# Kernel tuning notes

Hardware: AMD Instinct MI355X
Metric: run time of the kernel (lower is better)

Reference implementation:

```python
import jax, jax.numpy as jnp
import numpy as np

DIM = 180
WS = 16        # window_size
OWS = 24       # overlap_win_size = int(16*0.5)+16
HEADS = 6
HD = DIM // HEADS
MLP_HID = DIM * 2
TABLE = (WS + OWS - 1) ** 2  # 1521
H = W = 256
B = 1


def layernorm(x, g, b, eps=1e-5):
    mu = x.mean(-1, keepdims=True)
    d = x - mu
    var = (d * d).mean(-1, keepdims=True)
    return g * d / jnp.sqrt(var + eps) + b


def setup_inputs() -> dict:
    key = jax.random.key(0)
    ks = jax.random.split(key, 12)
    std = 0.02
    inp = {
        'x': jax.random.normal(ks[0], (B, H * W, DIM), jnp.float32),
        'rpi': jax.random.randint(ks[1], (WS * WS, OWS * OWS), 0, TABLE, jnp.int32),
        'h': H,
        'w': W,
        'norm1_g': jnp.ones((DIM,), jnp.float32),
        'norm1_b': jnp.zeros((DIM,), jnp.float32),
        'q_w': jax.random.normal(ks[2], (DIM, DIM), jnp.float32) * std,
        'q_b': jnp.zeros((DIM,), jnp.float32),
        'kv_w': jax.random.normal(ks[3], (DIM, 2 * DIM), jnp.float32) * std,
        'kv_b': jnp.zeros((2 * DIM,), jnp.float32),
        'rpb_table': jax.random.normal(ks[4], (TABLE, HEADS), jnp.float32) * std,
        'proj_w': jax.random.normal(ks[5], (DIM, DIM), jnp.float32) * std,
        'proj_b': jnp.zeros((DIM,), jnp.float32),
        'norm2_g': jnp.ones((DIM,), jnp.float32),
        'norm2_b': jnp.zeros((DIM,), jnp.float32),
        'mlp_w1': jax.random.normal(ks[6], (DIM, MLP_HID), jnp.float32) * std,
        'mlp_b1': jnp.zeros((MLP_HID,), jnp.float32),
        'mlp_w2': jax.random.normal(ks[7], (MLP_HID, DIM), jnp.float32) * std,
        'mlp_b2': jnp.zeros((DIM,), jnp.float32),
    }
    return inp


def reference(x, rpi, h, w, norm1_g, norm1_b, q_w, q_b, kv_w, kv_b,
              rpb_table, proj_w, proj_b, norm2_g, norm2_b,
              mlp_w1, mlp_b1, mlp_w2, mlp_b2):
    b, L, c = x.shape
    ws, ows, heads = WS, OWS, HEADS
    d = c // heads
    scale = d ** -0.5
    pad = (ows - ws) // 2  # 4
    nh, nw = h // ws, w // ws
    nq, n = ws * ws, ows * ows
    b_ = b * nh * nw

    shortcut = x
    xn = layernorm(x, norm1_g, norm1_b)
    x_img = xn.reshape(b, h, w, c)

    q = x_img @ q_w + q_b                    # [b,h,w,c]
    kv = x_img @ kv_w + kv_b                 # [b,h,w,2c] (k | v)

    # window_partition for q -> [b_, nq, c]
    qw = q.reshape(b, nh, ws, nw, ws, c).transpose(0, 1, 3, 2, 4, 5)
    qw = qw.reshape(b_, nq, c)

    # nn.Unfold(kernel=ows, stride=ws, padding=pad) on kv -> overlapping windows
    kvp = jnp.pad(kv, ((0, 0), (pad, pad), (pad, pad), (0, 0)))
    rows = (jnp.arange(nh) * ws)[:, None] + jnp.arange(ows)   # [nh, ows]
    cols = (jnp.arange(nw) * ws)[:, None] + jnp.arange(ows)   # [nw, ows]
    t = kvp[:, rows]                         # [b, nh, ows, W+2p, 2c]
    t = t[:, :, :, cols]                     # [b, nh, ows, nw, ows, 2c]
    t = t.transpose(0, 1, 3, 2, 4, 5).reshape(b_, n, 2 * c)
    k_win, v_win = t[..., :c], t[..., c:]

    qh = qw.reshape(b_, nq, heads, d).transpose(0, 2, 1, 3) * scale
    kh = k_win.reshape(b_, n, heads, d).transpose(0, 2, 1, 3)
    vh = v_win.reshape(b_, n, heads, d).transpose(0, 2, 1, 3)

    attn = jnp.einsum('bhqd,bhkd->bhqk', qh, kh)              # [b_,heads,nq,n]
    bias = rpb_table[rpi.reshape(-1)].reshape(nq, n, heads).transpose(2, 0, 1)
    attn = jax.nn.softmax(attn + bias[None], axis=-1)
    out = jnp.einsum('bhqk,bhkd->bhqd', attn, vh)
    out = out.transpose(0, 2, 1, 3).reshape(b_, nq, c)

    # window_reverse -> [b, h*w, c]
    xo = out.reshape(b, nh, nw, ws, ws, c).transpose(0, 1, 3, 2, 4, 5)
    xo = xo.reshape(b, h * w, c)

    xo = xo @ proj_w + proj_b + shortcut
    xn2 = layernorm(xo, norm2_g, norm2_b)
    mlp = jax.nn.gelu(xn2 @ mlp_w1 + mlp_b1, approximate=False) @ mlp_w2 + mlp_b2
    return xo + mlp
```

## Files before the change

### kernel.cpp

```cpp
#include <hip/hip_runtime.h>
#include <hip/hip_bf16.h>
#include <stdint.h>

#define DIM 180
#define WS 16
#define OWS 24
#define HEADS 6
#define HD 30
#define MLP_HID 360
#define HH 256
#define WW 256
#define L (HH * WW)
#define NWIN 256
#define NQ 256
#define NK 576

#define KP1 192
#define KP2 384
#define NQKV 576

#define QSCALE 0.2633988734672831f
#define LOG2E 1.4426950408889634f

typedef float f4v __attribute__((ext_vector_type(4)));
typedef short s8v __attribute__((ext_vector_type(8)));
typedef short s4v __attribute__((ext_vector_type(4)));

static __device__ __forceinline__ short f2bf(float x) {
    union { __hip_bfloat16 h; short s; } u;
    u.h = __float2bfloat16(x);
    return u.s;
}
static __device__ __forceinline__ uint32_t pack_bf2(float lo, float hi) {
    union { __hip_bfloat162 h; uint32_t u; } u;
    u.h.x = __float2bfloat16(lo);
    u.h.y = __float2bfloat16(hi);
    return u.u;
}
static __device__ __forceinline__ float bflo(uint32_t u) {
    union { uint32_t i; float f; } c; c.i = u << 16; return c.f;
}
static __device__ __forceinline__ float bfhi(uint32_t u) {
    union { uint32_t i; float f; } c; c.i = u & 0xffff0000u; return c.f;
}

typedef __attribute__((address_space(1))) const unsigned int ga_u32;
typedef __attribute__((address_space(3))) unsigned int la_u32;
static __device__ __forceinline__ void gld16(const void* g, void* l) {
    __builtin_amdgcn_global_load_lds((ga_u32*)g, (la_u32*)l, 16, 0, 0);
}

__global__ __launch_bounds__(64) void ln_kernel(const float* __restrict__ x,
                                                const float* __restrict__ g,
                                                const float* __restrict__ b,
                                                __hip_bfloat16* __restrict__ out) {
    int row = blockIdx.x;
    int t = threadIdx.x;
    const float* xr = x + (size_t)row * DIM;
    float v0 = xr[t];
    float v1 = xr[t + 64];
    float v2 = (t < DIM - 128) ? xr[t + 128] : 0.f;
    float s = v0 + v1 + v2;
    #pragma unroll
    for (int o = 32; o > 0; o >>= 1) s += __shfl_down(s, o);
    s = __shfl(s, 0);
    float mu = s * (1.f / DIM);
    float d0 = v0 - mu, d1 = v1 - mu;
    float d2 = (t < DIM - 128) ? (v2 - mu) : 0.f;
    float vs = d0 * d0 + d1 * d1 + d2 * d2;
    #pragma unroll
    for (int o = 32; o > 0; o >>= 1) vs += __shfl_down(vs, o);
    vs = __shfl(vs, 0);
    float rstd = rsqrtf(vs * (1.f / DIM) + 1e-5f);
    __hip_bfloat16* orow = out + (size_t)row * KP1;
    orow[t]      = __float2bfloat16(g[t] * d0 * rstd + b[t]);
    orow[t + 64] = __float2bfloat16(g[t + 64] * d1 * rstd + b[t + 64]);
    if (t < DIM - 128)
        orow[t + 128] = __float2bfloat16(g[t + 128] * d2 * rstd + b[t + 128]);
    if (t < KP1 - DIM) orow[DIM + t] = __float2bfloat16(0.f);
}

__global__ __launch_bounds__(256) void bias_kernel(const int* __restrict__ rpi,
                                                   const float* __restrict__ rpb,
                                                   ushort* __restrict__ biasC) {
    int idx = blockIdx.x * 256 + threadIdx.x;
    int j = idx & 15;
    int q = (idx >> 4) & 255;
    int r = idx >> 12;
    int kc = r % 36;
    int head = r / 36;
    int k = (kc >> 1) * 32 + ((j >> 2) << 3) + ((kc & 1) << 2) + (j & 3);
    int t = rpi[q * NK + k];
    biasC[idx] = (ushort)f2bf(rpb[t * HEADS + head] * LOG2E);
}

__global__ __launch_bounds__(256) void wconv_kernel(
        const float* __restrict__ qw, const float* __restrict__ kvw,
        const float* __restrict__ pw, const float* __restrict__ w1,
        const float* __restrict__ w2, short* __restrict__ wt) {
    int idx = blockIdx.x * 256 + threadIdx.x;
    float v = 0.f;
    if (idx < 110592) {
        int n = idx / KP1, k = idx - n * KP1;
        if (k < DIM) {
            if (n < DIM) v = qw[k * DIM + n] * QSCALE;
            else if (n < 540) v = kvw[k * (2 * DIM) + (n - DIM)];
        }
    } else if (idx < 147456) {
        int r = idx - 110592;
        int n = r / KP1, k = r - n * KP1;
        if (k < DIM && n < DIM) v = pw[k * DIM + n];
    } else if (idx < 221184) {
        int r = idx - 147456;
        int n = r / KP1, k = r - n * KP1;
        if (k < DIM && n < MLP_HID) v = w1[k * MLP_HID + n];
    } else {
        int r = idx - 221184;
        int n = r / KP2, k = r - n * KP2;
        if (k < MLP_HID && n < DIM) v = w2[k * DIM + n];
    }
    wt[idx] = f2bf(v);
}

__global__ __launch_bounds__(256) void bconv_kernel(
        const float* __restrict__ qb, const float* __restrict__ kvb,
        const float* __restrict__ pb, const float* __restrict__ b1,
        const float* __restrict__ b2, float* __restrict__ bv) {
    int idx = blockIdx.x * 256 + threadIdx.x;
    if (idx >= 1344) return;
    float v = 0.f;
    if (idx < 576) {
        if (idx < DIM) v = qb[idx] * QSCALE;
        else if (idx < 540) v = kvb[idx - DIM];
    } else if (idx < 768) {
        int n = idx - 576; if (n < DIM) v = pb[n];
    } else if (idx < 1152) {
        int n = idx - 768; if (n < MLP_HID) v = b1[n];
    } else {
        int n = idx - 1152; if (n < DIM) v = b2[n];
    }
    bv[idx] = v;
}

__global__ __launch_bounds__(256) void mgemm(
        const short* __restrict__ A, const short* __restrict__ Wt,
        const float* __restrict__ bias,
        float* __restrict__ outf, short* __restrict__ outb,
        int lda, int ldo, int nK, int mode) {
    __shared__ short As[2][128 * 32];
    __shared__ short Wsm[2][64 * 32];
    int tid = threadIdx.x;
    int lane = tid & 63, wave = tid >> 6;
    int q15 = lane & 15, quad = lane >> 4;
    int n0 = blockIdx.x * 64;
    int m0 = blockIdx.y * 128;

    auto stage = [&](int buf, int k0) {
        int lr = lane >> 2, c = lane & 3;
        const short* Ab = A + (size_t)m0 * lda + k0;
        #pragma unroll
        for (int i = 0; i < 2; i++) {
            int r = i * 64 + wave * 16 + lr;
            gld16(Ab + (size_t)r * lda + ((c ^ (r & 3)) * 8),
                  &As[buf][(i * 64 + wave * 16) * 32]);
        }
        const short* Wb = Wt + (size_t)n0 * lda + k0;
        {
            int r = wave * 16 + lr;
            gld16(Wb + (size_t)r * lda + ((c ^ (r & 3)) * 8),
                  &Wsm[buf][(wave * 16) * 32]);
        }
    };

    f4v acc[2][4];
    #pragma unroll
    for (int a = 0; a < 2; a++)
        #pragma unroll
        for (int b = 0; b < 4; b++) acc[a][b] = (f4v){0.f, 0.f, 0.f, 0.f};

    stage(0, 0);
    __syncthreads();
    for (int ch = 0; ch < nK; ch++) {
        int buf = ch & 1;
        if (ch + 1 < nK) stage(buf ^ 1, (ch + 1) * 32);
        s8v af[2], wf[4];
        #pragma unroll
        for (int mt = 0; mt < 2; mt++) {
            int r = wave * 32 + mt * 16 + q15;
            af[mt] = *(const s8v*)&As[buf][r * 32 + ((quad ^ (r & 3)) * 8)];
        }
        #pragma unroll
        for (int nt = 0; nt < 4; nt++) {
            int r = nt * 16 + q15;
            wf[nt] = *(const s8v*)&Wsm[buf][r * 32 + ((quad ^ (r & 3)) * 8)];
        }
        #pragma unroll
        for (int mt = 0; mt < 2; mt++)
            #pragma unroll
            for (int nt = 0; nt < 4; nt++)
                acc[mt][nt] = __builtin_amdgcn_mfma_f32_16x16x32_bf16(
                    af[mt], wf[nt], acc[mt][nt], 0, 0, 0);
        __syncthreads();
    }

    #pragma unroll
    for (int mt = 0; mt < 2; mt++) {
        int mb = m0 + wave * 32 + mt * 16 + quad * 4;
        #pragma unroll
        for (int nt = 0; nt < 4; nt++) {
            int n = n0 + nt * 16 + q15;
            float bv = bias[n];
            f4v a = acc[mt][nt];
            #pragma unroll
            for (int r = 0; r < 4; r++) {
                int m = mb + r;
                float v = a[r] + bv;
                if (mode == 0) {
                    outb[(size_t)m * ldo + n] = f2bf(v);
                } else if (mode == 1) {
                    float ge = 0.5f * v * (1.f + erff(v * 0.70710678118654752f));
                    outb[(size_t)m * ldo + n] = f2bf(ge);
                } else {
                    if (n < DIM) outf[(size_t)m * DIM + n] += v;
                }
            }
        }
    }
}

__global__ __launch_bounds__(256) void projln(
        const short* __restrict__ A, const short* __restrict__ Wt,
        const float* __restrict__ bias, const float* __restrict__ resid,
        const float* __restrict__ g2, const float* __restrict__ b2,
        float* __restrict__ outf, short* __restrict__ outb) {
    __shared__ short As[2][64 * 32];
    __shared__ short Wsm[2][192 * 32];
    int tid = threadIdx.x;
    int lane = tid & 63, wave = tid >> 6;
    int q15 = lane & 15, quad = lane >> 4;
    int m0 = blockIdx.x * 64;

    auto stage = [&](int buf, int k0) {
        int lr = lane >> 2, c = lane & 3;
        const short* Ab = A + (size_t)m0 * KP1 + k0;
        {
            int r = wave * 16 + lr;
            gld16(Ab + (size_t)r * KP1 + ((c ^ (r & 3)) * 8),
                  &As[buf][(wave * 16) * 32]);
        }
        #pragma unroll
        for (int i = 0; i < 3; i++) {
            int r = i * 64 + wave * 16 + lr;
            gld16(Wt + (size_t)r * KP1 + k0 + ((c ^ (r & 3)) * 8),
                  &Wsm[buf][(i * 64 + wave * 16) * 32]);
        }
    };

    f4v acc[12];
    #pragma unroll
    for (int b = 0; b < 12; b++) acc[b] = (f4v){0.f, 0.f, 0.f, 0.f};

    stage(0, 0);
    __syncthreads();
    for (int ch = 0; ch < KP1 / 32; ch++) {
        int buf = ch & 1;
        if (ch + 1 < KP1 / 32) stage(buf ^ 1, (ch + 1) * 32);
        int ra = wave * 16 + q15;
        s8v af = *(const s8v*)&As[buf][ra * 32 + ((quad ^ (ra & 3)) * 8)];
        #pragma unroll
        for (int nt = 0; nt < 12; nt++) {
            int r = nt * 16 + q15;
            s8v wf = *(const s8v*)&Wsm[buf][r * 32 + ((quad ^ (r & 3)) * 8)];
            acc[nt] = __builtin_amdgcn_mfma_f32_16x16x32_bf16(af, wf, acc[nt], 0, 0, 0);
        }
        __syncthreads();
    }

    float gv[12], bv[12], biasv[12];
    #pragma unroll
    for (int nt = 0; nt < 12; nt++) {
        int n = nt * 16 + q15;
        biasv[nt] = bias[n];
        gv[nt] = (n < DIM) ? g2[n] : 0.f;
        bv[nt] = (n < DIM) ? b2[n] : 0.f;
    }
    int mb = m0 + wave * 16 + quad * 4;
    #pragma unroll
    for (int r = 0; r < 4; r++) {
        int m = mb + r;
        float v[12];
        float s = 0.f, ss = 0.f;
        #pragma unroll
        for (int nt = 0; nt < 12; nt++) {
            int n = nt * 16 + q15;
            float x = acc[nt][r] + biasv[nt];
            if (n < DIM) x += resid[(size_t)m * DIM + n];
            else x = 0.f;
            v[nt] = x;
            s += x;
            ss += x * x;
        }
        #pragma unroll
        for (int o = 8; o > 0; o >>= 1) {
            s += __shfl_xor(s, o);
            ss += __shfl_xor(ss, o);
        }
        float mu = s * (1.f / DIM);
        float var = ss * (1.f / DIM) - mu * mu;
        float rstd = rsqrtf(var + 1e-5f);
        #pragma unroll
        for (int nt = 0; nt < 12; nt++) {
            int n = nt * 16 + q15;
            if (n < DIM) outf[(size_t)m * DIM + n] = v[nt];
            outb[(size_t)m * KP1 + n] = f2bf(gv[nt] * (v[nt] - mu) * rstd + bv[nt]);
        }
    }
}

#define CHUNK 32
#define NCHUNK (NK / CHUNK)

__global__ __launch_bounds__(512) void attn_kernel(
        const __hip_bfloat16* __restrict__ qkvb,
        const ushort* __restrict__ biasC, __hip_bfloat16* __restrict__ aout) {
    __shared__ __align__(16) short Ks[2][CHUNK][32];
    __shared__ __align__(16) short Vt[2][32][40];

    int tid = threadIdx.x;
    int lane = tid & 63;
    int wave = tid >> 6;
    int q15 = lane & 15;
    int quad = lane >> 4;
    int bid = blockIdx.x;
    int grp = bid / 48;
    int r48 = bid - grp * 48;
    int head = r48 >> 3;
    int win = grp * 8 + (r48 & 7);
    int bh = win >> 4, bw = win & 15;

    const uint32_t* kvd = (const uint32_t*)qkvb;

    s8v qf[2];
    #pragma unroll
    for (int qt = 0; qt < 2; qt++) {
        int q = wave * 32 + qt * 16 + q15;
        int qy = q >> 4, qx = q & 15;
        size_t pos = (size_t)(bh * WS + qy) * WW + (bw * WS + qx);
        const uint32_t* qp = kvd + pos * 288 + head * 15 + quad * 4;
        uint32_t w0 = qp[0], w1 = qp[1], w2 = qp[2], w3 = qp[3];
        union { uint32_t u[4]; s8v v; } cv;
        cv.u[0] = w0; cv.u[1] = w1; cv.u[2] = w2; cv.u[3] = w3;
        qf[qt] = cv.v;
    }
    if (head == 0 && tid < 256) {
        int qy = tid >> 4, qx = tid & 15;
        size_t pos = (size_t)(bh * WS + qy) * WW + (bw * WS + qx);
        uint2 z = make_uint2(0u, 0u);
        uint2* oz = (uint2*)(aout + pos * KP1 + DIM);
        oz[0] = z; oz[1] = z; oz[2] = z;
    }

    bool lowh = tid < 256;
    int t2 = lowh ? tid : tid - 256;
    int keyK = t2 >> 3, pK = t2 & 7;
    int keyV = t2 & 31, pp = t2 >> 5;
    int pKs = pK ^ (((keyK >> 3) & 3) << 1);

    auto rowbase = [&](int jk) -> const uint32_t* {
        int oy = jk / OWS, ox = jk - oy * OWS;
        int y = bh * WS - 4 + oy, x = bw * WS - 4 + ox;
        if ((unsigned)y < HH && (unsigned)x < WW)
            return kvd + ((size_t)y * WW + x) * 288;
        return nullptr;
    };
    auto loadKV = [&](int c0, uint32_t& a, uint32_t& b) {
        a = b = 0u;
        if (lowh) {
            const uint32_t* rk = rowbase(c0 + keyK);
            if (rk) {
                const uint32_t* kp = rk + 90 + head * 15 + pK * 2;
                a = kp[0];
                if (pK < 7) b = kp[1];
            }
        } else {
            const uint32_t* rv = rowbase(c0 + keyV);
            if (rv) {
                const uint32_t* vp = rv + 180 + head * 15 + pp * 2;
                a = vp[0];
                if (pp < 7) b = vp[1];
            }
        }
    };
    auto writeKV = [&](int bufi, uint32_t a, uint32_t b) {
        if (lowh) {
            *(uint2*)&Ks[bufi][keyK][pKs * 4] = make_uint2(a, b);
        } else {
            int d0 = pp * 4;
            Vt[bufi][d0][keyV]     = (short)(a & 0xffff);
            Vt[bufi][d0 + 1][keyV] = (short)(a >> 16);
            if (pp < 7) {
                Vt[bufi][d0 + 2][keyV] = (short)(b & 0xffff);
                Vt[bufi][d0 + 3][keyV] = (short)(b >> 16);
            } else {
                Vt[bufi][30][keyV] = (short)0x3F80;
                Vt[bufi][31][keyV] = 0;
            }
        }
    };

    const char* bBase = (const char*)biasC +
        ((size_t)head * (36 * 256 * 16) + (size_t)(wave * 32 + q15) * 16 + quad * 4) * 2;
    uint2 bb[2][2];
    auto loadBias = [&](int ch) {
        #pragma unroll
        for (int kt = 0; kt < 2; kt++)
            #pragma unroll
            for (int qt = 0; qt < 2; qt++)
                bb[kt][qt] = *(const uint2*)(bBase + (size_t)(ch * 2 + kt) * 8192 + qt * 512);
    };

    uint32_t aA, bA, aB, bB2;

    loadKV(0, aA, bA);
    loadKV(CHUNK, aB, bB2);
    loadBias(0);
    writeKV(0, aA, bA);
    __syncthreads();

    f4v oacc[2][2];
    #pragma unroll
    for (int a = 0; a < 2; a++)
        #pragma unroll
        for (int b = 0; b < 2; b++) oacc[a][b] = (f4v){0.f, 0.f, 0.f, 0.f};

    int pr = ((q15 & 12) << 1) | (q15 & 3);
    int rslot = (quad ^ (q15 >> 2)) * 8;

    auto body = [&](int ch, int bufR,
                    uint32_t& aR, uint32_t& bR, uint32_t& aW, uint32_t& bW) {
        s8v kf0 = *(const s8v*)&Ks[bufR][pr][rslot];
        s8v kf1 = *(const s8v*)&Ks[bufR][pr + 4][rslot];
        s8v va0 = *(const s8v*)&Vt[bufR][q15][quad * 8];
        s8v va1 = *(const s8v*)&Vt[bufR][16 + q15][quad * 8];

        f4v zf = (f4v){0.f, 0.f, 0.f, 0.f};
        f4v s0[2], s1[2];
        #pragma unroll
        for (int qt = 0; qt < 2; qt++) {
            s0[qt] = __builtin_amdgcn_mfma_f32_16x16x32_bf16(kf0, qf[qt], zf, 0, 0, 0);
            s1[qt] = __builtin_amdgcn_mfma_f32_16x16x32_bf16(kf1, qf[qt], zf, 0, 0, 0);
        }
        if (ch + 2 < NCHUNK) loadKV((ch + 2) * CHUNK, aR, bR);

        s8v pbv[2];
        #pragma unroll
        for (int qt = 0; qt < 2; qt++) {
            uint2 b0 = bb[0][qt], b1 = bb[1][qt];
            union { uint32_t u[4]; s8v v; } pk;
            pk.u[0] = pack_bf2(__builtin_amdgcn_exp2f(s0[qt][0] + bflo(b0.x)),
                               __builtin_amdgcn_exp2f(s0[qt][1] + bfhi(b0.x)));
            pk.u[1] = pack_bf2(__builtin_amdgcn_exp2f(s0[qt][2] + bflo(b0.y)),
                               __builtin_amdgcn_exp2f(s0[qt][3] + bfhi(b0.y)));
            pk.u[2] = pack_bf2(__builtin_amdgcn_exp2f(s1[qt][0] + bflo(b1.x)),
                               __builtin_amdgcn_exp2f(s1[qt][1] + bfhi(b1.x)));
            pk.u[3] = pack_bf2(__builtin_amdgcn_exp2f(s1[qt][2] + bflo(b1.y)),
                               __builtin_amdgcn_exp2f(s1[qt][3] + bfhi(b1.y)));
            pbv[qt] = pk.v;
        }
        if (ch + 1 < NCHUNK) loadBias(ch + 1);

        #pragma unroll
        for (int qt = 0; qt < 2; qt++) {
            oacc[0][qt] = __builtin_amdgcn_mfma_f32_16x16x32_bf16(va0, pbv[qt], oacc[0][qt], 0, 0, 0);
            oacc[1][qt] = __builtin_amdgcn_mfma_f32_16x16x32_bf16(va1, pbv[qt], oacc[1][qt], 0, 0, 0);
        }

        if (ch + 1 < NCHUNK) writeKV(bufR ^ 1, aW, bW);

        asm volatile("s_waitcnt lgkmcnt(0)" ::: "memory");
        __builtin_amdgcn_sched_barrier(0);
        __builtin_amdgcn_s_barrier();
    };

    #pragma unroll 1
    for (int t = 0; t < NCHUNK / 2; t++) {
        body(2 * t,     0, aA, bA, aB, bB2);
        body(2 * t + 1, 1, aB, bB2, aA, bA);
    }

    #pragma unroll
    for (int qt = 0; qt < 2; qt++) {
        float l = __shfl(oacc[1][qt][2], 48 | q15);
        float rl = 1.0f / l;
        int q = wave * 32 + qt * 16 + q15;
        int qy = q >> 4, qx = q & 15;
        size_t pos = (size_t)(bh * WS + qy) * WW + (bw * WS + qx);
        uint32_t* od = (uint32_t*)(aout + pos * KP1 + head * HD);
        int dh = quad * 2;
        f4v o0 = oacc[0][qt], o1 = oacc[1][qt];
        od[dh]     = pack_bf2(o0[0] * rl, o0[1] * rl);
        od[dh + 1] = pack_bf2(o0[2] * rl, o0[3] * rl);
        od[8 + dh] = pack_bf2(o1[0] * rl, o1[1] * rl);
        if (quad < 3)
            od[8 + dh + 1] = pack_bf2(o1[2] * rl, o1[3] * rl);
    }
}

extern "C" void kernel_launch(void* const* d_in, const int* in_sizes, int n_in,
                              void* d_out, int out_size, void* d_ws, size_t ws_size,
                              hipStream_t stream) {
    const float* x      = (const float*)d_in[0];
    const int*   rpi    = (const int*)d_in[1];
    const float* n1g    = (const float*)d_in[4];
    const float* n1b    = (const float*)d_in[5];
    const float* q_w    = (const float*)d_in[6];
    const float* q_b    = (const float*)d_in[7];
    const float* kv_w   = (const float*)d_in[8];
    const float* kv_b   = (const float*)d_in[9];
    const float* rpb    = (const float*)d_in[10];
    const float* proj_w = (const float*)d_in[11];
    const float* proj_b = (const float*)d_in[12];
    const float* n2g    = (const float*)d_in[13];
    const float* n2b    = (const float*)d_in[14];
    const float* w1     = (const float*)d_in[15];
    const float* b1     = (const float*)d_in[16];
    const float* w2     = (const float*)d_in[17];
    const float* b2     = (const float*)d_in[18];
    float* out = (float*)d_out;

    char* ws = (char*)d_ws;
    short* qkvb  = (short*)(ws);
    short* xn    = (short*)(ws + 75497472ull);
    ushort* biasC = (ushort*)(ws + 100663296ull);
    short* wt    = (short*)(ws + 104202240ull);
    short* wt_qkv  = wt;
    short* wt_proj = wt + 110592;
    short* wt_1    = wt + 147456;
    short* wt_2    = wt + 221184;
    float* bvec  = (float*)(ws + 104202240ull + 589824ull);
    float* b_qkv  = bvec;
    float* b_proj = bvec + 576;
    float* b_1    = bvec + 768;
    float* b_2    = bvec + 1152;
    short* ao  = xn;
    short* xn2 = qkvb;
    short* h1  = qkvb + 12582912;

    bias_kernel<<<884736 / 256, 256, 0, stream>>>(rpi, rpb, biasC);
    wconv_kernel<<<294912 / 256, 256, 0, stream>>>(q_w, kv_w, proj_w, w1, w2, wt);
    bconv_kernel<<<6, 256, 0, stream>>>(q_b, kv_b, proj_b, b1, b2, bvec);
    ln_kernel<<<L, 64, 0, stream>>>(x, n1g, n1b, (__hip_bfloat16*)xn);
    mgemm<<<dim3(NQKV / 64, L / 128), 256, 0, stream>>>(
        xn, wt_qkv, b_qkv, nullptr, qkvb, KP1, NQKV, KP1 / 32, 0);
    attn_kernel<<<NWIN * HEADS, 512, 0, stream>>>(
        (const __hip_bfloat16*)qkvb, biasC, (__hip_bfloat16*)ao);
    projln<<<L / 64, 256, 0, stream>>>(
        ao, wt_proj, b_proj, x, n2g, n2b, out, xn2);
    mgemm<<<dim3(KP2 / 64, L / 128), 256, 0, stream>>>(
        xn2, wt_1, b_1, nullptr, h1, KP1, KP2, KP1 / 32, 1);
    mgemm<<<dim3(KP1 / 64, L / 128), 256, 0, stream>>>(
        h1, wt_2, b_2, out, nullptr, KP2, 0, KP2 / 32, 3);
}
```

Measured before the change: 396.7 us.

## Batch LN rows per block, swizzle GEMM block order, use tanh GELU

The layernorm kernel now processes four rows per 256-thread block instead of one row per 64-thread block, which cuts block launch overhead. The GEMM uses a flattened 1D grid remapped into groups of eight M-tiles per column sweep, to improve L2 reuse of A and W tiles. The exact erf GELU in the MLP epilogue is replaced with the tanh approximation computed via exp2. That approximation differs slightly from the reference's exact GELU and may affect accuracy tolerance.

```diff
diff --git a/kernel.cpp b/kernel.cpp
--- a/kernel.cpp
+++ b/kernel.cpp
@@ -50,12 +50,12 @@
     __builtin_amdgcn_global_load_lds((ga_u32*)g, (la_u32*)l, 16, 0, 0);
 }
 
-__global__ __launch_bounds__(64) void ln_kernel(const float* __restrict__ x,
-                                                const float* __restrict__ g,
-                                                const float* __restrict__ b,
-                                                __hip_bfloat16* __restrict__ out) {
-    int row = blockIdx.x;
-    int t = threadIdx.x;
+__global__ __launch_bounds__(256) void ln_kernel(const float* __restrict__ x,
+                                                 const float* __restrict__ g,
+                                                 const float* __restrict__ b,
+                                                 __hip_bfloat16* __restrict__ out) {
+    int row = blockIdx.x * 4 + (threadIdx.x >> 6);
+    int t = threadIdx.x & 63;
     const float* xr = x + (size_t)row * DIM;
     float v0 = xr[t];
     float v1 = xr[t + 64];
@@ -146,14 +146,19 @@
         const short* __restrict__ A, const short* __restrict__ Wt,
         const float* __restrict__ bias,
         float* __restrict__ outf, short* __restrict__ outb,
-        int lda, int ldo, int nK, int mode) {
+        int lda, int ldo, int nK, int mode, int nx) {
     __shared__ short As[2][128 * 32];
     __shared__ short Wsm[2][64 * 32];
     int tid = threadIdx.x;
     int lane = tid & 63, wave = tid >> 6;
     int q15 = lane & 15, quad = lane >> 4;
-    int n0 = blockIdx.x * 64;
-    int m0 = blockIdx.y * 128;
+    int bid = blockIdx.x;
+    int yl = bid & 7;
+    int h = bid >> 3;
+    int xx = h % nx;
+    int y = (h / nx) * 8 + yl;
+    int n0 = xx * 64;
+    int m0 = y * 128;
 
     auto stage = [&](int buf, int k0) {
         int lr = lane >> 2, c = lane & 3;
@@ -218,8 +223,10 @@
                 if (mode == 0) {
                     outb[(size_t)m * ldo + n] = f2bf(v);
                 } else if (mode == 1) {
-                    float ge = 0.5f * v * (1.f + erff(v * 0.70710678118654752f));
-                    outb[(size_t)m * ldo + n] = f2bf(ge);
+                    float y2 = 0.7978845608028654f * (v + 0.044715f * v * v * v);
+                    float e = __builtin_amdgcn_exp2f(y2 * 2.885390081777927f);
+                    float th = 1.f - 2.f / (1.f + e);
+                    outb[(size_t)m * ldo + n] = f2bf(0.5f * v * (1.f + th));
                 } else {
                     if (n < DIM) outf[(size_t)m * DIM + n] += v;
                 }
@@ -549,15 +556,15 @@
     bias_kernel<<<884736 / 256, 256, 0, stream>>>(rpi, rpb, biasC);
     wconv_kernel<<<294912 / 256, 256, 0, stream>>>(q_w, kv_w, proj_w, w1, w2, wt);
     bconv_kernel<<<6, 256, 0, stream>>>(q_b, kv_b, proj_b, b1, b2, bvec);
-    ln_kernel<<<L, 64, 0, stream>>>(x, n1g, n1b, (__hip_bfloat16*)xn);
-    mgemm<<<dim3(NQKV / 64, L / 128), 256, 0, stream>>>(
-        xn, wt_qkv, b_qkv, nullptr, qkvb, KP1, NQKV, KP1 / 32, 0);
+    ln_kernel<<<L / 4, 256, 0, stream>>>(x, n1g, n1b, (__hip_bfloat16*)xn);
+    mgemm<<<(NQKV / 64) * (L / 128), 256, 0, stream>>>(
+        xn, wt_qkv, b_qkv, nullptr, qkvb, KP1, NQKV, KP1 / 32, 0, NQKV / 64);
     attn_kernel<<<NWIN * HEADS, 512, 0, stream>>>(
         (const __hip_bfloat16*)qkvb, biasC, (__hip_bfloat16*)ao);
     projln<<<L / 64, 256, 0, stream>>>(
         ao, wt_proj, b_proj, x, n2g, n2b, out, xn2);
-    mgemm<<<dim3(KP2 / 64, L / 128), 256, 0, stream>>>(
-        xn2, wt_1, b_1, nullptr, h1, KP1, KP2, KP1 / 32, 1);
-    mgemm<<<dim3(KP1 / 64, L / 128), 256, 0, stream>>>(
-        h1, wt_2, b_2, out, nullptr, KP2, 0, KP2 / 32, 3);
-}
+    mgemm<<<(KP2 / 64) * (L / 128), 256, 0, stream>>>(
+        xn2, wt_1, b_1, nullptr, h1, KP1, KP2, KP1 / 32, 1, KP2 / 64);
+    mgemm<<<(KP1 / 64) * (L / 128), 256, 0, stream>>>(
+        h1, wt_2, b_2, out, nullptr, KP2, 0, KP2 / 32, 3, KP1 / 64);
+}
```

Measured after the change: 359.8 us. -9.3%, faster.
